# Optimization experiments

Measured on AMD Instinct MI355X. Metric: run time of the kernel, lower is better.

Reference implementation:

```python
import jax, jax.numpy as jnp
import numpy as np

B, NI, NO = 32, 64, 64


def setup_inputs() -> dict:
    key = jax.random.key(0)
    k1, k2, k3, k4, k5, k6 = jax.random.split(key, 6)
    return {
        "input_re": jax.random.normal(k1, (B, NI, NI), dtype=jnp.float32),
        "input_im": jax.random.normal(k2, (B, NI, NI), dtype=jnp.float32),
        "w_re": jax.random.normal(k3, (NI, NI, NO, NO), dtype=jnp.float32),
        "w_im": jax.random.normal(k4, (NI, NI, NO, NO), dtype=jnp.float32),
        "amp_weights": jax.random.normal(k5, (NI, NI), dtype=jnp.float32),
        "phase_weights": jax.random.normal(k6, (NI, NI), dtype=jnp.float32),
    }


def reference(input_re, input_im, w_re, w_im, amp_weights, phase_weights):
    # complex input field (B, NI, NI) and diffraction kernel (NI, NI, NO, NO)
    e_in = jax.lax.complex(input_re, input_im)
    w_ip = jax.lax.complex(w_re, w_im)
    # passive transmission coefficients: sigmoid(amp) * exp(i*phase)
    ts = (jax.nn.sigmoid(amp_weights)
          * jnp.exp(1j * phase_weights.astype(jnp.complex64))).astype(jnp.complex64)
    # modulated field, then sum over input pixels (i,j) -> complex GEMM
    modulated = e_in * ts[None, :, :]                    # (B, NI, NI)
    out = jnp.einsum('bij,ijkl->bkl', modulated, w_ip)   # (B, NO, NO)
    return out
```

## Files before the change

kernel.cpp:

```cpp
#include <hip/hip_runtime.h>
#include <cstdint>
#include <cstddef>

#define KC 4096
#define NN 4096
#define NB 32
#define HALF (NB * NN)

typedef __attribute__((ext_vector_type(8))) short  bf16x8;
typedef __attribute__((ext_vector_type(16))) float f32x16;

__device__ __forceinline__ uint32_t f2bf(float f) {
    union { float f; unsigned u; } v; v.f = f;
    unsigned r = v.u + 0x7fffu + ((v.u >> 16) & 1u);
    return r >> 16;
}

__global__ __launch_bounds__(256) void prep_kernel(
    const float* __restrict__ in_re, const float* __restrict__ in_im,
    const float* __restrict__ amp,   const float* __restrict__ phase,
    uint32_t* __restrict__ wsA)
{
    int tid = blockIdx.x * 256 + threadIdx.x;
    int b = tid >> 12;
    int k = tid & (KC - 1);
    float er = in_re[tid], ei = in_im[tid];
    float a = amp[k], p = phase[k];
    float s = 1.0f / (1.0f + expf(-a));
    float sn, cs;
    sincosf(p, &sn, &cs);
    float tr = s * cs, ti = s * sn;
    float mr = er * tr - ei * ti;
    float mi = er * ti + ei * tr;
    uint32_t pk = f2bf(mr) | (f2bf(mi) << 16);
    wsA[((((k >> 2) << 5) + b) << 2) | (k & 3)] = pk;
}

__global__ __launch_bounds__(256, 4) void gemm_kernel(
    const float* __restrict__ w_re, const float* __restrict__ w_im,
    const bf16x8* __restrict__ wsA, float2* __restrict__ wsP, int steps)
{
    const int lane = threadIdx.x & 63;
    const int wave = threadIdx.x >> 6;
    const int h    = lane >> 5;
    const int l32  = lane & 31;
    const int n    = blockIdx.x * 128 + wave * 32 + l32;
    const int s    = blockIdx.y;
    const int kbase = s * (steps * 8);

    f32x16 accR = {};
    f32x16 accI = {};

    const bf16x8* aptr = wsA + ((size_t)(kbase >> 2) + h) * 32 + l32;
    const float* pre = w_re + (size_t)(kbase + h * 4) * NN + n;
    const float* pim = w_im + (size_t)(kbase + h * 4) * NN + n;

    bf16x8 af = aptr[0];
    float r0 = pre[0], r1 = pre[NN], r2 = pre[2 * NN], r3 = pre[3 * NN];
    float i0 = pim[0], i1 = pim[NN], i2 = pim[2 * NN], i3 = pim[3 * NN];

    for (int t = 0; t < steps - 1; ++t) {
        bf16x8 afn = aptr[(size_t)(2 * (t + 1)) * 32];
        const float* prn = pre + (size_t)(t + 1) * 8 * NN;
        const float* pin = pim + (size_t)(t + 1) * 8 * NN;
        float r0n = prn[0], r1n = prn[NN], r2n = prn[2 * NN], r3n = prn[3 * NN];
        float i0n = pin[0], i1n = pin[NN], i2n = pin[2 * NN], i3n = pin[3 * NN];

        uint32_t R0 = f2bf(r0), R1 = f2bf(r1), R2 = f2bf(r2), R3 = f2bf(r3);
        uint32_t I0 = f2bf(i0), I1 = f2bf(i1), I2 = f2bf(i2), I3 = f2bf(i3);
        union { bf16x8 v; uint32_t d[4]; } uR, uI;
        uR.d[0] = R0 | ((I0 ^ 0x8000u) << 16);  uI.d[0] = I0 | (R0 << 16);
        uR.d[1] = R1 | ((I1 ^ 0x8000u) << 16);  uI.d[1] = I1 | (R1 << 16);
        uR.d[2] = R2 | ((I2 ^ 0x8000u) << 16);  uI.d[2] = I2 | (R2 << 16);
        uR.d[3] = R3 | ((I3 ^ 0x8000u) << 16);  uI.d[3] = I3 | (R3 << 16);
        accR = __builtin_amdgcn_mfma_f32_32x32x16_bf16(af, uR.v, accR, 0, 0, 0);
        accI = __builtin_amdgcn_mfma_f32_32x32x16_bf16(af, uI.v, accI, 0, 0, 0);

        af = afn;
        r0 = r0n; r1 = r1n; r2 = r2n; r3 = r3n;
        i0 = i0n; i1 = i1n; i2 = i2n; i3 = i3n;
    }

    {
        uint32_t R0 = f2bf(r0), R1 = f2bf(r1), R2 = f2bf(r2), R3 = f2bf(r3);
        uint32_t I0 = f2bf(i0), I1 = f2bf(i1), I2 = f2bf(i2), I3 = f2bf(i3);
        union { bf16x8 v; uint32_t d[4]; } uR, uI;
        uR.d[0] = R0 | ((I0 ^ 0x8000u) << 16);  uI.d[0] = I0 | (R0 << 16);
        uR.d[1] = R1 | ((I1 ^ 0x8000u) << 16);  uI.d[1] = I1 | (R1 << 16);
        uR.d[2] = R2 | ((I2 ^ 0x8000u) << 16);  uI.d[2] = I2 | (R2 << 16);
        uR.d[3] = R3 | ((I3 ^ 0x8000u) << 16);  uI.d[3] = I3 | (R3 << 16);
        accR = __builtin_amdgcn_mfma_f32_32x32x16_bf16(af, uR.v, accR, 0, 0, 0);
        accI = __builtin_amdgcn_mfma_f32_32x32x16_bf16(af, uI.v, accI, 0, 0, 0);
    }

#pragma unroll
    for (int r = 0; r < 16; ++r) {
        int brow = (r & 3) + 8 * (r >> 2) + 4 * h;
        float2 v; v.x = accR[r]; v.y = accI[r];
        wsP[((size_t)s * NB + brow) * NN + n] = v;
    }
}

__global__ __launch_bounds__(256) void reduce_kernel(
    const float2* __restrict__ wsP, float* __restrict__ out, int S)
{
    int tid = blockIdx.x * 256 + threadIdx.x;
    float re = 0.f, im = 0.f;
    for (int s = 0; s < S; ++s) {
        float2 v = wsP[(size_t)s * (NB * NN) + tid];
        re += v.x; im += v.y;
    }
    out[tid]        = re;
    out[HALF + tid] = im;
}

extern "C" void kernel_launch(void* const* d_in, const int* in_sizes, int n_in,
                              void* d_out, int out_size, void* d_ws, size_t ws_size,
                              hipStream_t stream)
{
    const float* in_re  = (const float*)d_in[0];
    const float* in_im  = (const float*)d_in[1];
    const float* w_re   = (const float*)d_in[2];
    const float* w_im   = (const float*)d_in[3];
    const float* amp    = (const float*)d_in[4];
    const float* phase  = (const float*)d_in[5];

    const size_t A_BYTES = (size_t)1024 * 32 * 16;
    uint32_t* wsA = (uint32_t*)d_ws;
    float2*   wsP = (float2*)((char*)d_ws + A_BYTES);

    int S = 32;
    while (S > 1 && A_BYTES + (size_t)S * NB * NN * sizeof(float2) > ws_size) S >>= 1;
    int steps = (KC / S) / 8;

    prep_kernel<<<dim3((NB * KC) / 256), dim3(256), 0, stream>>>(
        in_re, in_im, amp, phase, wsA);

    gemm_kernel<<<dim3(NN / 128, S), dim3(256), 0, stream>>>(
        w_re, w_im, (const bf16x8*)wsA, wsP, steps);

    reduce_kernel<<<dim3((NB * NN) / 256), dim3(256), 0, stream>>>(
        wsP, (float*)d_out, S);
}
```

Before: 174.0 us.

## Stage weight tiles into LDS via direct global-to-LDS loads per K chunk

The GEMM kernel now copies each 32-row K chunk of w_re/w_im into shared memory with global_load_lds 16-byte transfers, waits, syncs, then reads the values from LDS to build bf16 MFMA operands. Before, each lane did scalar global loads with one-step register prefetch. The aim is wider, coalesced memory transactions for the dominant 128MB weight stream. The cost is full-barrier synchronisation per chunk with no double buffering, so load and compute no longer overlap within a block. The split count is also hardcoded to 32, dropping the workspace-size fallback.

```diff
diff --git a/kernel.cpp b/kernel.cpp
--- a/kernel.cpp
+++ b/kernel.cpp
@@ -6,6 +6,11 @@
 #define NN 4096
 #define NB 32
 #define HALF (NB * NN)
+#define S_SPLIT 32
+#define KSP (KC / S_SPLIT)
+#define CK 32
+#define NCHUNK (KSP / CK)
+#define CSTEPS (CK / 8)
 
 typedef __attribute__((ext_vector_type(8))) short  bf16x8;
 typedef __attribute__((ext_vector_type(16))) float f32x16;
@@ -14,6 +19,12 @@
     union { float f; unsigned u; } v; v.f = f;
     unsigned r = v.u + 0x7fffu + ((v.u >> 16) & 1u);
     return r >> 16;
+}
+
+__device__ __forceinline__ void load_lds16(const float* g, float* lds) {
+    __builtin_amdgcn_global_load_lds(
+        (const __attribute__((address_space(1))) void*)g,
+        (__attribute__((address_space(3))) void*)lds, 16, 0, 0);
 }
 
 __global__ __launch_bounds__(256) void prep_kernel(
@@ -38,59 +49,69 @@
 
 __global__ __launch_bounds__(256, 4) void gemm_kernel(
     const float* __restrict__ w_re, const float* __restrict__ w_im,
-    const bf16x8* __restrict__ wsA, float2* __restrict__ wsP, int steps)
+    const bf16x8* __restrict__ wsA, float2* __restrict__ wsP)
 {
+    __shared__ float shW[2 * CK * 128];
     const int lane = threadIdx.x & 63;
     const int wave = threadIdx.x >> 6;
     const int h    = lane >> 5;
     const int l32  = lane & 31;
-    const int n    = blockIdx.x * 128 + wave * 32 + l32;
+    const int c32  = wave * 32 + l32;
+    const int n0   = blockIdx.x * 128;
+    const int n    = n0 + c32;
     const int s    = blockIdx.y;
-    const int kbase = s * (steps * 8);
+    const int kbase = s * KSP;
 
-    f32x16 accR = {};
-    f32x16 accI = {};
+    const int srow = lane >> 5;
+    const int scol = (lane & 31) * 4;
 
-    const bf16x8* aptr = wsA + ((size_t)(kbase >> 2) + h) * 32 + l32;
-    const float* pre = w_re + (size_t)(kbase + h * 4) * NN + n;
-    const float* pim = w_im + (size_t)(kbase + h * 4) * NN + n;
+    f32x16 accR = {}, accI = {};
 
-    bf16x8 af = aptr[0];
-    float r0 = pre[0], r1 = pre[NN], r2 = pre[2 * NN], r3 = pre[3 * NN];
-    float i0 = pim[0], i1 = pim[NN], i2 = pim[2 * NN], i3 = pim[3 * NN];
+#pragma unroll
+    for (int c = 0; c < NCHUNK; ++c) {
+        bf16x8 a[CSTEPS];
+#pragma unroll
+        for (int st = 0; st < CSTEPS; ++st) {
+            int m = c * CSTEPS + st;
+            a[st] = wsA[((size_t)(kbase >> 2) + 2 * m + h) * 32 + l32];
+        }
 
-    for (int t = 0; t < steps - 1; ++t) {
-        bf16x8 afn = aptr[(size_t)(2 * (t + 1)) * 32];
-        const float* prn = pre + (size_t)(t + 1) * 8 * NN;
-        const float* pin = pim + (size_t)(t + 1) * 8 * NN;
-        float r0n = prn[0], r1n = prn[NN], r2n = prn[2 * NN], r3n = prn[3 * NN];
-        float i0n = pin[0], i1n = pin[NN], i2n = pin[2 * NN], i3n = pin[3 * NN];
+        const int krow0 = kbase + c * CK;
+#pragma unroll
+        for (int i = 0; i < 8; ++i) {
+            int seg = wave * 8 + i;
+            const float* wp = (seg < 16) ? w_re : w_im;
+            int rp = seg & 15;
+            const float* g = wp + (size_t)(krow0 + 2 * rp + srow) * NN
+                                + (n0 + scol);
+            load_lds16(g, &shW[seg * 256]);
+        }
+        asm volatile("s_waitcnt vmcnt(0)" ::: "memory");
+        __syncthreads();
 
-        uint32_t R0 = f2bf(r0), R1 = f2bf(r1), R2 = f2bf(r2), R3 = f2bf(r3);
-        uint32_t I0 = f2bf(i0), I1 = f2bf(i1), I2 = f2bf(i2), I3 = f2bf(i3);
-        union { bf16x8 v; uint32_t d[4]; } uR, uI;
-        uR.d[0] = R0 | ((I0 ^ 0x8000u) << 16);  uI.d[0] = I0 | (R0 << 16);
-        uR.d[1] = R1 | ((I1 ^ 0x8000u) << 16);  uI.d[1] = I1 | (R1 << 16);
-        uR.d[2] = R2 | ((I2 ^ 0x8000u) << 16);  uI.d[2] = I2 | (R2 << 16);
-        uR.d[3] = R3 | ((I3 ^ 0x8000u) << 16);  uI.d[3] = I3 | (R3 << 16);
-        accR = __builtin_amdgcn_mfma_f32_32x32x16_bf16(af, uR.v, accR, 0, 0, 0);
-        accI = __builtin_amdgcn_mfma_f32_32x32x16_bf16(af, uI.v, accI, 0, 0, 0);
+#pragma unroll
+        for (int st = 0; st < CSTEPS; ++st) {
+            int rb = st * 8 + h * 4;
+            float r0 = shW[(rb + 0) * 128 + c32];
+            float r1 = shW[(rb + 1) * 128 + c32];
+            float r2 = shW[(rb + 2) * 128 + c32];
+            float r3 = shW[(rb + 3) * 128 + c32];
+            float i0 = shW[4096 + (rb + 0) * 128 + c32];
+            float i1 = shW[4096 + (rb + 1) * 128 + c32];
+            float i2 = shW[4096 + (rb + 2) * 128 + c32];
+            float i3 = shW[4096 + (rb + 3) * 128 + c32];
 
-        af = afn;
-        r0 = r0n; r1 = r1n; r2 = r2n; r3 = r3n;
-        i0 = i0n; i1 = i1n; i2 = i2n; i3 = i3n;
-    }
-
-    {
-        uint32_t R0 = f2bf(r0), R1 = f2bf(r1), R2 = f2bf(r2), R3 = f2bf(r3);
-        uint32_t I0 = f2bf(i0), I1 = f2bf(i1), I2 = f2bf(i2), I3 = f2bf(i3);
-        union { bf16x8 v; uint32_t d[4]; } uR, uI;
-        uR.d[0] = R0 | ((I0 ^ 0x8000u) << 16);  uI.d[0] = I0 | (R0 << 16);
-        uR.d[1] = R1 | ((I1 ^ 0x8000u) << 16);  uI.d[1] = I1 | (R1 << 16);
-        uR.d[2] = R2 | ((I2 ^ 0x8000u) << 16);  uI.d[2] = I2 | (R2 << 16);
-        uR.d[3] = R3 | ((I3 ^ 0x8000u) << 16);  uI.d[3] = I3 | (R3 << 16);
-        accR = __builtin_amdgcn_mfma_f32_32x32x16_bf16(af, uR.v, accR, 0, 0, 0);
-        accI = __builtin_amdgcn_mfma_f32_32x32x16_bf16(af, uI.v, accI, 0, 0, 0);
+            uint32_t R0 = f2bf(r0), R1 = f2bf(r1), R2 = f2bf(r2), R3 = f2bf(r3);
+            uint32_t I0 = f2bf(i0), I1 = f2bf(i1), I2 = f2bf(i2), I3 = f2bf(i3);
+            union { bf16x8 v; uint32_t d[4]; } uR, uI;
+            uR.d[0] = R0 | ((I0 ^ 0x8000u) << 16);  uI.d[0] = I0 | (R0 << 16);
+            uR.d[1] = R1 | ((I1 ^ 0x8000u) << 16);  uI.d[1] = I1 | (R1 << 16);
+            uR.d[2] = R2 | ((I2 ^ 0x8000u) << 16);  uI.d[2] = I2 | (R2 << 16);
+            uR.d[3] = R3 | ((I3 ^ 0x8000u) << 16);  uI.d[3] = I3 | (R3 << 16);
+            accR = __builtin_amdgcn_mfma_f32_32x32x16_bf16(a[st], uR.v, accR, 0, 0, 0);
+            accI = __builtin_amdgcn_mfma_f32_32x32x16_bf16(a[st], uI.v, accI, 0, 0, 0);
+        }
+        __syncthreads();
     }
 
 #pragma unroll
@@ -129,16 +150,12 @@
     uint32_t* wsA = (uint32_t*)d_ws;
     float2*   wsP = (float2*)((char*)d_ws + A_BYTES);
 
-    int S = 32;
-    while (S > 1 && A_BYTES + (size_t)S * NB * NN * sizeof(float2) > ws_size) S >>= 1;
-    int steps = (KC / S) / 8;
-
     prep_kernel<<<dim3((NB * KC) / 256), dim3(256), 0, stream>>>(
         in_re, in_im, amp, phase, wsA);
 
-    gemm_kernel<<<dim3(NN / 128, S), dim3(256), 0, stream>>>(
-        w_re, w_im, (const bf16x8*)wsA, wsP, steps);
+    gemm_kernel<<<dim3(NN / 128, S_SPLIT), dim3(256), 0, stream>>>(
+        w_re, w_im, (const bf16x8*)wsA, wsP);
 
     reduce_kernel<<<dim3((NB * NN) / 256), dim3(256), 0, stream>>>(
-        wsP, (float*)d_out, S);
+        wsP, (float*)d_out, S_SPLIT);
 }
```

After: 173.0 us. About the same (-0.6%).
